# Performance work log

Hardware: AMD Instinct MI355X
Metric: run time of the kernel (lower is better)

Reference implementation:

```python
import jax, jax.numpy as jnp
from jax import lax
import numpy as np

# SafetyChecker constants (hard-coded defaults in the torch module)
H, W = 48, 80
MPPX = 40.0 / W   # 0.5 m/px
MPPY = 30.0 / H   # 0.625 m/px
CX, CY = W // 2, H // 2  # 40, 24
# collision window half sizes: int((ego/2 + margin)/mpp)
COL_HW = int((2.0 / 2 + 1.0) / MPPX)  # 4
COL_HL = int((4.5 / 2 + 1.0) / MPPY)  # 5
# lane window half sizes: int((ego/2)/mpp)
LANE_HW = int(2.0 / 2 / MPPX)  # 2
LANE_HL = int(4.5 / 2 / MPPY)  # 3

W_TRAJ, W_COL, W_LANE, W_SMOOTH, W_CONF = 1.0, 5.0, 2.0, 0.5, 0.1


def _to_pixels(traj):
    # traj: [B, S, 2] meters -> int pixel coords, clamped (truncation matches .long())
    px = jnp.clip((traj[..., 0] / MPPX + CX).astype(jnp.int32), 0, W - 1)
    py = jnp.clip((traj[..., 1] / MPPY + CY).astype(jnp.int32), 0, H - 1)
    return px, py


def _collision_risk(traj, det_mask):
    # windowed max over a (2*COL_HL+1) x (2*COL_HW+1) box, truncated at edges
    px, py = _to_pixels(traj)  # [B, S]
    pooled = lax.reduce_window(
        det_mask, -jnp.inf, lax.max,
        window_dimensions=(1, 2 * COL_HL + 1, 2 * COL_HW + 1),
        window_strides=(1, 1, 1),
        padding=((0, 0), (COL_HL, COL_HL), (COL_HW, COL_HW)))
    b = jnp.arange(det_mask.shape[0])[:, None]
    return pooled[b, py, px]  # [B, S]


def _lane_compliance(traj, driv_mask):
    # windowed mean over clamped box via integral image
    px, py = _to_pixels(traj)
    x_min = jnp.maximum(px - LANE_HW, 0)
    x_max = jnp.minimum(px + LANE_HW + 1, W)
    y_min = jnp.maximum(py - LANE_HL, 0)
    y_max = jnp.minimum(py + LANE_HL + 1, H)
    ii = jnp.pad(jnp.cumsum(jnp.cumsum(driv_mask, axis=1), axis=2),
                 ((0, 0), (1, 0), (1, 0)))  # [B, H+1, W+1]
    b = jnp.arange(driv_mask.shape[0])[:, None]
    box_sum = (ii[b, y_max, x_max] - ii[b, y_min, x_max]
               - ii[b, y_max, x_min] + ii[b, y_min, x_min])
    count = ((y_max - y_min) * (x_max - x_min)).astype(driv_mask.dtype)
    return box_sum / count  # [B, S]


def setup_inputs() -> dict:
    key = jax.random.key(0)
    k1, k2, k3, k4, k5 = jax.random.split(key, 5)
    B, S = 8192, 6
    # scale so trajectories span a good fraction of the 40m x 30m BEV
    pred_traj = jax.random.normal(k1, (B, S, 2), jnp.float32) * 6.0
    targ_traj = jax.random.normal(k2, (B, S, 2), jnp.float32) * 6.0
    conf = jax.random.uniform(k3, (B, S), jnp.float32)
    det_mask = (jax.random.uniform(k4, (B, H, W), jnp.float32) > 0.9).astype(jnp.float32)
    driv_mask = (jax.random.uniform(k5, (B, H, W), jnp.float32) > 0.3).astype(jnp.float32)
    return {"predicted_trajectory": pred_traj,
            "predicted_confidence": conf,
            "target_trajectory": targ_traj,
            "detection_mask": det_mask,
            "drivable_area_mask": driv_mask}


def reference(predicted_trajectory, predicted_confidence, target_trajectory,
              detection_mask, drivable_area_mask):
    # trajectory MSE
    traj_loss = jnp.mean((predicted_trajectory - target_trajectory) ** 2)
    # collision
    collision_risks = _collision_risk(predicted_trajectory, detection_mask)
    collision_loss = jnp.mean(collision_risks)
    # lane keeping
    lane_compliance = _lane_compliance(predicted_trajectory, drivable_area_mask)
    lane_keeping_loss = jnp.mean(1.0 - lane_compliance)
    # smoothness (second difference L2 norm)
    velocity = predicted_trajectory[:, 1:] - predicted_trajectory[:, :-1]
    acceleration = velocity[:, 1:] - velocity[:, :-1]
    smoothness_loss = jnp.mean(jnp.linalg.norm(acceleration, axis=-1))
    # confidence MSE against (1 - collision risk)
    confidence_loss = jnp.mean((predicted_confidence - (1.0 - collision_risks)) ** 2)
    total_loss = (W_TRAJ * traj_loss + W_COL * collision_loss
                  + W_LANE * lane_keeping_loss + W_SMOOTH * smoothness_loss
                  + W_CONF * confidence_loss)
    return total_loss
```

## Files before the change

kernel.cpp:

```cpp
#include <hip/hip_runtime.h>
#include <math.h>


#define MH 48
#define MW 80
#define TS 6

__global__ __launch_bounds__(256) void planning_partial(
    const float* __restrict__ pred,
    const float* __restrict__ conf,
    const float* __restrict__ targ,
    const float* __restrict__ det,
    const float* __restrict__ driv,
    float* __restrict__ partials,
    int B)
{
    const int lane   = threadIdx.x & 63;
    const int widblk = threadIdx.x >> 6;
    const int gwid   = blockIdx.x * 4 + widblk;
    const int NW     = B * TS;

    float partial = 0.0f;

    if (gwid < NW) {
        const int b = gwid / TS;
        const int s = gwid - b * TS;

        const float x = pred[(b * TS + s) * 2 + 0];
        const float y = pred[(b * TS + s) * 2 + 1];

        int px = (int)(x * 2.0f + 40.0f);
        int py = (int)(y / 0.625f + 24.0f);
        px = min(max(px, 0), MW - 1);
        py = min(max(py, 0), MH - 1);

        const size_t mbase = (size_t)b * (MH * MW);

        float m = -INFINITY;
        #pragma unroll
        for (int it = 0; it < 2; ++it) {
            int e = lane + it * 64;
            if (e < 99) {
                int r  = e / 9;
                int dy = r - 5;
                int dx = (e - r * 9) - 4;
                int yy = py + dy, xx = px + dx;
                if (yy >= 0 && yy < MH && xx >= 0 && xx < MW)
                    m = fmaxf(m, det[mbase + yy * MW + xx]);
            }
        }
        #pragma unroll
        for (int o = 32; o > 0; o >>= 1)
            m = fmaxf(m, __shfl_xor(m, o));

        float ssum = 0.0f;
        if (lane < 35) {
            int r  = lane / 5;
            int dy = r - 3;
            int dx = (lane - r * 5) - 2;
            int yy = py + dy, xx = px + dx;
            if (yy >= 0 && yy < MH && xx >= 0 && xx < MW)
                ssum = driv[mbase + yy * MW + xx];
        }
        #pragma unroll
        for (int o = 32; o > 0; o >>= 1)
            ssum += __shfl_xor(ssum, o);

        if (lane == 0) {
            int ymin = max(py - 3, 0), ymax = min(py + 4, MH);
            int xmin = max(px - 2, 0), xmax = min(px + 3, MW);
            float cnt  = (float)((ymax - ymin) * (xmax - xmin));
            float comp = ssum / cnt;

            float tx = x - targ[(b * TS + s) * 2 + 0];
            float ty = y - targ[(b * TS + s) * 2 + 1];
            float sq = tx * tx + ty * ty;

            float sm = 0.0f;
            if (s >= 1 && s <= TS - 2) {
                float xm = pred[(b * TS + s - 1) * 2 + 0];
                float ym = pred[(b * TS + s - 1) * 2 + 1];
                float xp = pred[(b * TS + s + 1) * 2 + 0];
                float yp = pred[(b * TS + s + 1) * 2 + 1];
                float ax = (xp - x) - (x - xm);
                float ay = (yp - y) - (y - ym);
                sm = sqrtf(ax * ax + ay * ay);
            }

            float c  = conf[b * TS + s];
            float ce = c - (1.0f - m);
            ce = ce * ce;

            const float invBS = 1.0f / (float)NW;
            partial = sq * (1.0f * 0.5f * invBS)
                    + m  * (5.0f * invBS)
                    + (1.0f - comp) * (2.0f * invBS)
                    + sm * (0.5f / (float)(B * (TS - 2)))
                    + ce * (0.1f * invBS);
        }
    }

    __shared__ float red[4];
    if (lane == 0) red[widblk] = partial;
    __syncthreads();
    if (threadIdx.x == 0)
        partials[blockIdx.x] = (red[0] + red[1]) + (red[2] + red[3]);
}

__global__ __launch_bounds__(256) void planning_reduce(
    const float* __restrict__ partials, int n, float* __restrict__ out)
{
    __shared__ float red[256];
    float s = 0.0f;
    for (int i = threadIdx.x; i < n; i += 256)
        s += partials[i];
    red[threadIdx.x] = s;
    __syncthreads();
    #pragma unroll
    for (int o = 128; o > 0; o >>= 1) {
        if (threadIdx.x < o) red[threadIdx.x] += red[threadIdx.x + o];
        __syncthreads();
    }
    if (threadIdx.x == 0) out[0] = red[0];
}

extern "C" void kernel_launch(void* const* d_in, const int* in_sizes, int n_in,
                              void* d_out, int out_size, void* d_ws, size_t ws_size,
                              hipStream_t stream) {
    const float* pred = (const float*)d_in[0];
    const float* conf = (const float*)d_in[1];
    const float* targ = (const float*)d_in[2];
    const float* det  = (const float*)d_in[3];
    const float* driv = (const float*)d_in[4];

    const int B    = in_sizes[3] / (MH * MW);
    const int nw   = B * TS;
    const int nblk = (nw + 3) / 4;

    float* partials = (float*)d_ws;

    planning_partial<<<nblk, 256, 0, stream>>>(pred, conf, targ, det, driv,
                                               partials, B);
    planning_reduce<<<1, 256, 0, stream>>>(partials, nblk, (float*)d_out);
}
```

Before: 248.4 us.

## Process all trajectory steps of a batch element in one wavefront

Work is remapped from one wavefront per (batch, step) pair to one wavefront per batch element. Each wave loads pred, targ and conf once with a few lanes and broadcasts them by shuffle. It then issues all six steps' windowed gathers on the detection and drivable masks before any of the reductions. The aim is to cut the wave count and redundant scalar loads, and to raise memory-level parallelism on these latency-bound gathers. In exchange each thread uses more registers, and there are six times fewer waves to hide latency.

```diff
diff --git a/kernel.cpp b/kernel.cpp
--- a/kernel.cpp
+++ b/kernel.cpp
@@ -15,93 +15,103 @@
     float* __restrict__ partials,
     int B)
 {
-    const int lane   = threadIdx.x & 63;
-    const int widblk = threadIdx.x >> 6;
-    const int gwid   = blockIdx.x * 4 + widblk;
-    const int NW     = B * TS;
+    const int lane = threadIdx.x & 63;
+    const int wid  = threadIdx.x >> 6;
+    const int b    = blockIdx.x * 4 + wid;
 
     float partial = 0.0f;
 
-    if (gwid < NW) {
-        const int b = gwid / TS;
-        const int s = gwid - b * TS;
+    if (b < B) {
+        const float pv = (lane < 12) ? pred[b * 12 + lane] : 0.0f;
+        const float tv = (lane < 12) ? targ[b * 12 + lane] : 0.0f;
+        const float cv = (lane < 6)  ? conf[b * 6 + lane]  : 0.0f;
 
-        const float x = pred[(b * TS + s) * 2 + 0];
-        const float y = pred[(b * TS + s) * 2 + 1];
+        float xs[TS], ys[TS];
+        int   px[TS], py[TS];
+        #pragma unroll
+        for (int s = 0; s < TS; ++s) {
+            xs[s] = __shfl(pv, 2 * s);
+            ys[s] = __shfl(pv, 2 * s + 1);
+            int ix = (int)(xs[s] * 2.0f + 40.0f);
+            int iy = (int)(ys[s] / 0.625f + 24.0f);
+            px[s] = min(max(ix, 0), MW - 1);
+            py[s] = min(max(iy, 0), MH - 1);
+        }
 
-        int px = (int)(x * 2.0f + 40.0f);
-        int py = (int)(y / 0.625f + 24.0f);
-        px = min(max(px, 0), MW - 1);
-        py = min(max(py, 0), MH - 1);
+        const float* img = det  + (size_t)b * (MH * MW);
+        const float* drv = driv + (size_t)b * (MH * MW);
 
-        const size_t mbase = (size_t)b * (MH * MW);
-
-        float m = -INFINITY;
+        float mA[TS], mB[TS], dv[TS];
         #pragma unroll
-        for (int it = 0; it < 2; ++it) {
-            int e = lane + it * 64;
-            if (e < 99) {
-                int r  = e / 9;
-                int dy = r - 5;
-                int dx = (e - r * 9) - 4;
-                int yy = py + dy, xx = px + dx;
-                if (yy >= 0 && yy < MH && xx >= 0 && xx < MW)
-                    m = fmaxf(m, det[mbase + yy * MW + xx]);
+        for (int s = 0; s < TS; ++s) {
+            {
+                int e = lane, r = e / 9;
+                int yy = py[s] + r - 5, xx = px[s] + (e - 9 * r) - 4;
+                mA[s] = (yy >= 0 && yy < MH && xx >= 0 && xx < MW)
+                      ? img[yy * MW + xx] : -INFINITY;
+            }
+            {
+                int e = lane + 35, r = e / 9;
+                int yy = py[s] + r - 5, xx = px[s] + (e - 9 * r) - 4;
+                mB[s] = (yy >= 0 && yy < MH && xx >= 0 && xx < MW)
+                      ? img[yy * MW + xx] : -INFINITY;
+            }
+            {
+                int e = lane, r = e / 5;
+                int yy = py[s] + r - 3, xx = px[s] + (e - 5 * r) - 2;
+                dv[s] = (lane < 35 && yy >= 0 && yy < MH && xx >= 0 && xx < MW)
+                      ? drv[yy * MW + xx] : 0.0f;
             }
         }
+
+        float col[TS], lsum[TS];
         #pragma unroll
-        for (int o = 32; o > 0; o >>= 1)
-            m = fmaxf(m, __shfl_xor(m, o));
+        for (int s = 0; s < TS; ++s) {
+            float m = fmaxf(mA[s], mB[s]);
+            float d = dv[s];
+            #pragma unroll
+            for (int o = 32; o > 0; o >>= 1) {
+                m = fmaxf(m, __shfl_xor(m, o));
+                d += __shfl_xor(d, o);
+            }
+            col[s]  = m;
+            lsum[s] = d;
+        }
 
-        float ssum = 0.0f;
-        if (lane < 35) {
-            int r  = lane / 5;
-            int dy = r - 3;
-            int dx = (lane - r * 5) - 2;
-            int yy = py + dy, xx = px + dx;
-            if (yy >= 0 && yy < MH && xx >= 0 && xx < MW)
-                ssum = driv[mbase + yy * MW + xx];
+        float diff = pv - tv;
+        float sq = diff * diff;
+        #pragma unroll
+        for (int o = 32; o > 0; o >>= 1) sq += __shfl_xor(sq, o);
+
+        float colsum = 0.0f, ce = 0.0f, lanec = 0.0f;
+        #pragma unroll
+        for (int s = 0; s < TS; ++s) {
+            colsum += col[s];
+            float c = __shfl(cv, s);
+            float e = c - (1.0f - col[s]);
+            ce += e * e;
+            int ymin = max(py[s] - 3, 0), ymax = min(py[s] + 4, MH);
+            int xmin = max(px[s] - 2, 0), xmax = min(px[s] + 3, MW);
+            lanec += 1.0f - lsum[s] / (float)((ymax - ymin) * (xmax - xmin));
         }
+        float sm = 0.0f;
         #pragma unroll
-        for (int o = 32; o > 0; o >>= 1)
-            ssum += __shfl_xor(ssum, o);
+        for (int s = 1; s <= TS - 2; ++s) {
+            float ax = (xs[s + 1] - xs[s]) - (xs[s] - xs[s - 1]);
+            float ay = (ys[s + 1] - ys[s]) - (ys[s] - ys[s - 1]);
+            sm += sqrtf(ax * ax + ay * ay);
+        }
 
-        if (lane == 0) {
-            int ymin = max(py - 3, 0), ymax = min(py + 4, MH);
-            int xmin = max(px - 2, 0), xmax = min(px + 3, MW);
-            float cnt  = (float)((ymax - ymin) * (xmax - xmin));
-            float comp = ssum / cnt;
-
-            float tx = x - targ[(b * TS + s) * 2 + 0];
-            float ty = y - targ[(b * TS + s) * 2 + 1];
-            float sq = tx * tx + ty * ty;
-
-            float sm = 0.0f;
-            if (s >= 1 && s <= TS - 2) {
-                float xm = pred[(b * TS + s - 1) * 2 + 0];
-                float ym = pred[(b * TS + s - 1) * 2 + 1];
-                float xp = pred[(b * TS + s + 1) * 2 + 0];
-                float yp = pred[(b * TS + s + 1) * 2 + 1];
-                float ax = (xp - x) - (x - xm);
-                float ay = (yp - y) - (y - ym);
-                sm = sqrtf(ax * ax + ay * ay);
-            }
-
-            float c  = conf[b * TS + s];
-            float ce = c - (1.0f - m);
-            ce = ce * ce;
-
-            const float invBS = 1.0f / (float)NW;
-            partial = sq * (1.0f * 0.5f * invBS)
-                    + m  * (5.0f * invBS)
-                    + (1.0f - comp) * (2.0f * invBS)
-                    + sm * (0.5f / (float)(B * (TS - 2)))
-                    + ce * (0.1f * invBS);
-        }
+        const float invBS = 1.0f / (float)(B * TS);
+        partial = sq     * (1.0f * 0.5f * invBS)
+                + colsum * (5.0f * invBS)
+                + lanec  * (2.0f * invBS)
+                + sm     * (0.5f / (float)(B * (TS - 2)))
+                + ce     * (0.1f * invBS);
     }
 
     __shared__ float red[4];
-    if (lane == 0) red[widblk] = partial;
+    if (lane == 0) red[wid] = partial;
     __syncthreads();
     if (threadIdx.x == 0)
         partials[blockIdx.x] = (red[0] + red[1]) + (red[2] + red[3]);
@@ -134,8 +144,7 @@
     const float* driv = (const float*)d_in[4];
 
     const int B    = in_sizes[3] / (MH * MW);
-    const int nw   = B * TS;
-    const int nblk = (nw + 3) / 4;
+    const int nblk = (B + 3) / 4;
 
     float* partials = (float*)d_ws;
 
```

Measured after the change: 238.4 us. 1.04x faster.
